# Kernel optimization log

Measured on AMD Instinct MI355X. Metric: run time of the kernel, lower is better.

The kernel has to match this reference:

```python
import math
from itertools import product
import jax, jax.numpy as jnp
import numpy as np

# ---- static config (mirrors LPD.__init__) ----
IMG_W, IMG_H = 1920, 1080
MIN_SIZES = [[10, 16, 24], [32, 48], [64, 96], [128, 192, 256]]
STEPS = [8, 16, 32, 64]
VARIANCE = (0.1, 0.2)
CONF_THR = 0.3
NMS_THR = 0.3
TOP_K = 2000
KEEP_TOP_K = 750
BATCH = 16


def make_priors() -> np.ndarray:
    """Anchor grid in normalized (cx, cy, w, h), kornia _PriorBox order:
    per level, per cell (row-major), per min_size."""
    levels = []
    for step, mss in zip(STEPS, MIN_SIZES):
        fh, fw = math.ceil(IMG_H / step), math.ceil(IMG_W / step)
        ii, jj = np.meshgrid(np.arange(fh), np.arange(fw), indexing='ij')
        cx = (jj + 0.5) * step / IMG_W  # [fh, fw]
        cy = (ii + 0.5) * step / IMG_H
        nms_ = len(mss)
        cx = np.broadcast_to(cx[..., None], (fh, fw, nms_))
        cy = np.broadcast_to(cy[..., None], (fh, fw, nms_))
        skx = np.broadcast_to(np.array(mss, np.float64) / IMG_W, (fh, fw, nms_))
        sky = np.broadcast_to(np.array(mss, np.float64) / IMG_H, (fh, fw, nms_))
        levels.append(np.stack([cx, cy, skx, sky], -1).reshape(-1, 4))
    return np.concatenate(levels, 0).astype(np.float32)  # [N, 4]

N_PRIORS = make_priors().shape[0]  # 119130 for 1920x1080


def decode(loc, priors):
    """loc [B,N,14], priors [N,4] -> scaled [B,N,14] (x1y1x2y2 + 5 landmarks)."""
    var = jnp.asarray(VARIANCE, loc.dtype)
    p_xy, p_wh = priors[:, :2], priors[:, 2:4]
    cxcy = p_xy + loc[..., 0:2] * VARIANCE[0] * p_wh
    wh = p_wh * jnp.exp(loc[..., 2:4] * var)
    x1y1 = cxcy - wh * 0.5
    x2y2 = x1y1 + wh
    # 5 landmark points
    lmk = p_xy[None, :, None, :] + loc[..., 4:14].reshape(*loc.shape[:-1], 5, 2) * VARIANCE[0] * p_wh[None, :, None, :]
    boxes = jnp.concatenate([x1y1, x2y2, lmk.reshape(*loc.shape[:-1], 10)], -1)
    scale = jnp.tile(jnp.asarray([IMG_W, IMG_H], loc.dtype), 7)
    return boxes * scale


def nms_keep(b, s):
    """Greedy NMS. b [K,4] sorted by descending score s [K]. Returns bool keep [K]."""
    area = jnp.clip(b[:, 2] - b[:, 0], 0.0) * jnp.clip(b[:, 3] - b[:, 1], 0.0)
    lt = jnp.maximum(b[:, None, :2], b[None, :, :2])
    rb = jnp.minimum(b[:, None, 2:4], b[None, :, 2:4])
    whi = jnp.clip(rb - lt, 0.0)
    inter = whi[..., 0] * whi[..., 1]
    iou_m = inter / (area[:, None] + area[None, :] - inter + 1e-9)  # [K,K]
    K = b.shape[0]
    idx = jnp.arange(K)

    def step(active, i):
        keep_i = active[i]
        active = active & ~(keep_i & (iou_m[i] > NMS_THR) & (idx > i))
        return active, keep_i

    _, keep = jax.lax.scan(step, s > 0.0, idx)
    return keep


def setup_inputs() -> dict:
    key = jax.random.key(0)
    k1, k2, k3 = jax.random.split(key, 3)
    return {
        'loc': jax.random.normal(k1, (BATCH, N_PRIORS, 14), jnp.float32),
        'conf': jax.random.normal(k2, (BATCH, N_PRIORS, 2), jnp.float32),
        'iou': jax.random.normal(k3, (BATCH, N_PRIORS, 1), jnp.float32),
    }


def reference(loc, conf, iou):
    priors = jnp.asarray(make_priors())  # [N,4] constant
    cls = jax.nn.softmax(conf, axis=-1)[..., 1]          # [B,N]
    iou_s = jnp.clip(iou[..., 0], 0.0, 1.0)
    scores = jnp.sqrt(cls * iou_s)
    scores = jnp.where(scores >= CONF_THR, scores, 0.0)  # confidence threshold
    boxes = decode(loc, priors)                          # [B,N,14]
    top_s, top_i = jax.lax.top_k(scores, TOP_K)          # sorted desc
    boxes_k = jnp.take_along_axis(boxes, top_i[..., None], axis=1)  # [B,K,14]
    keep = jax.vmap(nms_keep)(boxes_k[..., :4], top_s)   # [B,K] bool
    keep = keep & (jnp.cumsum(keep.astype(jnp.int32), axis=-1) <= KEEP_TOP_K)
    dets = jnp.concatenate([boxes_k, (top_s * keep)[..., None]], -1)  # [B,K,15]
    return dets
```

## Files before the change

kernel.cpp:

```cpp
#include <hip/hip_runtime.h>
#include <math.h>

#define BB 16
#define TOPK 2000
#define KEEPK 750
#define CAND_CAP 4096
#define EDGE_CAP 8192
#define HIST_BINS 256
#define BIN_BASE 0x3E99u

#define OFF_HIST   0
#define OFF_CCOUNT 16384
#define OFF_ECOUNT 16448
#define ZERO_BYTES 16512
#define OFF_SBITS  16512

__global__ __launch_bounds__(256) void k_scores(const float* __restrict__ conf,
                                                const float* __restrict__ iou,
                                                unsigned* __restrict__ sbits,
                                                unsigned* __restrict__ hist, int N) {
  __shared__ unsigned h[HIST_BINS];
  int b = blockIdx.y;
  for (int i = threadIdx.x; i < HIST_BINS; i += blockDim.x) h[i] = 0;
  __syncthreads();
  const float2* c2 = (const float2*)conf + (size_t)b * N;
  const float* iu = iou + (size_t)b * N;
  unsigned* sb = sbits + (size_t)b * N;
  int n0 = blockIdx.x * 4096;
#pragma unroll 4
  for (int k = 0; k < 16; ++k) {
    int n = n0 + k * 256 + threadIdx.x;
    if (n < N) {
      float2 c = c2[n];
      float m = fmaxf(c.x, c.y);
      float e0 = (float)exp((double)(c.x - m));
      float e1 = (float)exp((double)(c.y - m));
      float p1 = e1 / (e0 + e1);
      float ic = fminf(fmaxf(iu[n], 0.0f), 1.0f);
      float s = sqrtf(p1 * ic);
      s = (s >= 0.3f) ? s : 0.0f;
      unsigned bits = __float_as_uint(s);
      sb[n] = bits;
      if (bits != 0u) {
        int bin = (int)(bits >> 16) - (int)BIN_BASE;
        bin = bin < 0 ? 0 : (bin > 255 ? 255 : bin);
        atomicAdd(&h[bin], 1u);
      }
    }
  }
  __syncthreads();
  for (int i = threadIdx.x; i < HIST_BINS; i += blockDim.x)
    if (h[i]) atomicAdd(&hist[b * HIST_BINS + i], h[i]);
}

__global__ __launch_bounds__(256) void k_compact(const unsigned* __restrict__ sbits,
                                                 const unsigned* __restrict__ hist,
                                                 unsigned* __restrict__ ccount,
                                                 unsigned long long* __restrict__ ckeys,
                                                 int N) {
  __shared__ unsigned sT;
  __shared__ unsigned long long masks[32];
  __shared__ unsigned wioff[32];
  __shared__ unsigned blockbase;
  int b = blockIdx.y;
  int tid = threadIdx.x, lane = tid & 63, wv = tid >> 6;

  if (tid < 64) {
    const unsigned* h = hist + b * HIST_BINS;
    unsigned v0 = h[255 - (4 * lane + 0)];
    unsigned v1 = h[255 - (4 * lane + 1)];
    unsigned v2 = h[255 - (4 * lane + 2)];
    unsigned v3 = h[255 - (4 * lane + 3)];
    unsigned p0 = v0, p1 = p0 + v1, p2 = p1 + v2, p3 = p2 + v3;
    unsigned tot = p3, pre = tot;
    for (int off = 1; off < 64; off <<= 1) {
      unsigned q = __shfl_up(pre, off);
      if (lane >= off) pre += q;
    }
    unsigned excl = pre - tot;
    int kk = -1;
    if (excl + p0 >= TOPK) kk = 0;
    else if (excl + p1 >= TOPK) kk = 1;
    else if (excl + p2 >= TOPK) kk = 2;
    else if (excl + p3 >= TOPK) kk = 3;
    unsigned long long m = __ballot(kk >= 0);
    int bin = 0;
    if (m != 0ull) {
      int fl = __ffsll((unsigned long long)m) - 1;
      int fk = __shfl(kk, fl);
      bin = 255 - (4 * fl + fk);
    }
    if (lane == 0) sT = ((unsigned)(BIN_BASE + (unsigned)bin)) << 16;
  }
  __syncthreads();
  unsigned T = sT;

  const unsigned* sb = sbits + (size_t)b * N;
  int n0 = blockIdx.x * 2048;
  unsigned v[8];
  unsigned long long mk[8];
#pragma unroll
  for (int k = 0; k < 8; ++k) {
    int n = n0 + k * 256 + tid;
    v[k] = (n < N) ? sb[n] : 0u;
    bool p = v[k] >= T;
    mk[k] = __ballot(p);
    if (lane == 0) masks[k * 4 + wv] = mk[k];
  }
  __syncthreads();
  if (tid < 64) {
    unsigned c = (tid < 32) ? (unsigned)__popcll(masks[tid]) : 0u;
    unsigned pre = c;
    for (int off = 1; off < 64; off <<= 1) {
      unsigned q = __shfl_up(pre, off);
      if (lane >= off) pre += q;
    }
    if (tid < 32) wioff[tid] = pre - c;
    if (tid == 31) blockbase = atomicAdd(&ccount[b], pre);
  }
  __syncthreads();
  unsigned base = blockbase;
#pragma unroll
  for (int k = 0; k < 8; ++k) {
    if ((mk[k] >> lane) & 1ull) {
      unsigned pos = base + wioff[k * 4 + wv] +
                     (unsigned)__popcll(mk[k] & ((1ull << lane) - 1ull));
      if (pos < CAND_CAP) {
        int n = n0 + k * 256 + tid;
        ckeys[(size_t)b * CAND_CAP + pos] =
            ((unsigned long long)v[k] << 32) | (unsigned)(~(unsigned)n);
      }
    }
  }
}

__global__ __launch_bounds__(1024) void k_sort_decode(
    const unsigned* __restrict__ ccount, const unsigned long long* __restrict__ ckeys,
    const float* __restrict__ loc, float* __restrict__ top_s,
    float* __restrict__ out, float4* __restrict__ boxes4, int N) {
  __shared__ unsigned long long s[CAND_CAP];
  int b = blockIdx.x;
  int t = threadIdx.x;
  unsigned c = ccount[b];
  if (c > CAND_CAP) c = CAND_CAP;
  const unsigned long long* src = ckeys + (size_t)b * CAND_CAP;
  unsigned long long key[4];
#pragma unroll
  for (int e = 0; e < 4; ++e) {
    int i = 4 * t + e;
    key[e] = (i < (int)c) ? src[i] : 0ull;
  }
  for (int k = 2; k <= CAND_CAP; k <<= 1) {
    for (int j = k >> 1; j > 0; j >>= 1) {
      if (j >= 256) {
        __syncthreads();
#pragma unroll
        for (int e = 0; e < 4; ++e) s[4 * t + e] = key[e];
        __syncthreads();
        int pbase = (4 * t) ^ j;
        bool own_lo = ((4 * t) & j) == 0;
        bool dir = ((4 * t) & k) == 0;
        bool keep_max = (own_lo == dir);
#pragma unroll
        for (int e = 0; e < 4; ++e) {
          unsigned long long o = s[pbase + e];
          unsigned long long mx = key[e] > o ? key[e] : o;
          unsigned long long mn = key[e] > o ? o : key[e];
          key[e] = keep_max ? mx : mn;
        }
      } else if (j >= 4) {
        int d = j >> 2;
        bool own_lo = (t & d) == 0;
        bool dir = ((4 * t) & k) == 0;
        bool keep_max = (own_lo == dir);
#pragma unroll
        for (int e = 0; e < 4; ++e) {
          unsigned long long o = __shfl_xor(key[e], d, 64);
          unsigned long long mx = key[e] > o ? key[e] : o;
          unsigned long long mn = key[e] > o ? o : key[e];
          key[e] = keep_max ? mx : mn;
        }
      } else {
#pragma unroll
        for (int e = 0; e < 4; ++e) {
          int p = e ^ j;
          if (p > e) {
            int i = 4 * t + e;
            bool dir = ((i & k) == 0);
            bool need = dir ? (key[e] < key[p]) : (key[e] > key[p]);
            if (need) { unsigned long long tmp = key[e]; key[e] = key[p]; key[p] = tmp; }
          }
        }
      }
    }
  }
  if (t < TOPK / 4) {
#pragma unroll
    for (int e = 0; e < 4; ++e) {
      int r = 4 * t + e;
      unsigned long long kk = key[e];
      float sv = __uint_as_float((unsigned)(kk >> 32));
      top_s[b * TOPK + r] = sv;
      unsigned idxu = ~(unsigned)kk;
      if (idxu >= (unsigned)N) idxu = 0;
      int i = (int)idxu;
      int off, fw, st, nm, lvl;
      if (i < 97200)       { lvl = 0; off = 0;      fw = 240; st = 8;  nm = 3; }
      else if (i < 113520) { lvl = 1; off = 97200;  fw = 120; st = 16; nm = 2; }
      else if (i < 117600) { lvl = 2; off = 113520; fw = 60;  st = 32; nm = 2; }
      else                 { lvl = 3; off = 117600; fw = 30;  st = 64; nm = 3; }
      int tt = i - off;
      int cell = tt / nm;
      int kms = tt - cell * nm;
      int row = cell / fw;
      int col = cell - row * fw;
      int msv = (lvl == 0) ? (kms == 0 ? 10 : (kms == 1 ? 16 : 24))
              : (lvl == 1) ? (kms == 0 ? 32 : 48)
              : (lvl == 2) ? (kms == 0 ? 64 : 96)
                           : (kms == 0 ? 128 : (kms == 1 ? 192 : 256));
      float cx  = (float)(((double)col + 0.5) * (double)st / 1920.0);
      float cy  = (float)(((double)row + 0.5) * (double)st / 1080.0);
      float skx = (float)((double)msv / 1920.0);
      float sky = (float)((double)msv / 1080.0);
      const float2* lp2 = (const float2*)(loc + ((size_t)b * N + (size_t)i) * 14);
      float l[14];
#pragma unroll
      for (int q = 0; q < 7; ++q) { float2 v = lp2[q]; l[2 * q] = v.x; l[2 * q + 1] = v.y; }
      float cx2 = cx + (l[0] * 0.1f) * skx;
      float cy2 = cy + (l[1] * 0.1f) * sky;
      float wx = skx * expf(l[2] * 0.1f);
      float wy = sky * expf(l[3] * 0.2f);
      float x1 = cx2 - wx * 0.5f, y1 = cy2 - wy * 0.5f;
      float x2 = x1 + wx, y2 = y1 + wy;
      float X1 = x1 * 1920.0f, Y1 = y1 * 1080.0f, X2 = x2 * 1920.0f, Y2 = y2 * 1080.0f;
      float* o = out + ((size_t)b * TOPK + r) * 15;
      o[0] = X1; o[1] = Y1; o[2] = X2; o[3] = Y2;
#pragma unroll
      for (int q = 0; q < 5; ++q) {
        o[4 + 2 * q] = (cx + (l[4 + 2 * q] * 0.1f) * skx) * 1920.0f;
        o[5 + 2 * q] = (cy + (l[5 + 2 * q] * 0.1f) * sky) * 1080.0f;
      }
      boxes4[b * TOPK + r] = make_float4(X1, Y1, X2, Y2);
    }
  }
}

__global__ __launch_bounds__(256) void k_edges(const float4* __restrict__ boxes4,
                                               unsigned* __restrict__ ecount,
                                               unsigned* __restrict__ edges) {
  __shared__ float4 cb[256];
  __shared__ unsigned loc_e[1024];
  __shared__ unsigned lcnt, gbase;
  int b = blockIdx.y;
  int t = blockIdx.x;
  int ib = 0;
  while ((ib + 1) * (ib + 2) / 2 <= t) ++ib;
  int jb = t - ib * (ib + 1) / 2;
  int tid = threadIdx.x;
  if (tid == 0) lcnt = 0;
  int j0 = jb * 256;
  {
    int j = j0 + tid;
    cb[tid] = (j < TOPK) ? boxes4[b * TOPK + j]
                         : make_float4(-1e30f, -1e30f, -1e30f, -1e30f);
  }
  __syncthreads();
  int r = ib * 256 + tid;
  bool valid = r < TOPK;
  float4 A = valid ? boxes4[b * TOPK + r] : make_float4(0, 0, 0, 0);
  float areaA = fmaxf(A.z - A.x, 0.f) * fmaxf(A.w - A.y, 0.f);
  int cmax = r - j0;
  if (cmax > 256) cmax = 256;
  if (!valid) cmax = 0;
  for (int c = 0; c < cmax; ++c) {
    float4 Bx = cb[c];
    float xx1 = fmaxf(A.x, Bx.x), yy1 = fmaxf(A.y, Bx.y);
    float xx2 = fminf(A.z, Bx.z), yy2 = fminf(A.w, Bx.w);
    float w = fmaxf(xx2 - xx1, 0.f), hgt = fmaxf(yy2 - yy1, 0.f);
    float inter = w * hgt;
    float areaB = fmaxf(Bx.z - Bx.x, 0.f) * fmaxf(Bx.w - Bx.y, 0.f);
    float iouv = inter / (areaA + areaB - inter + 1e-9f);
    if (iouv > 0.3f) {
      unsigned p = atomicAdd(&lcnt, 1u);
      if (p < 1024u) loc_e[p] = ((unsigned)r << 16) | (unsigned)(j0 + c);
    }
  }
  __syncthreads();
  unsigned cnt = lcnt;
  if (cnt > 1024u) cnt = 1024u;
  if (tid == 0 && cnt) gbase = atomicAdd(&ecount[b], cnt);
  __syncthreads();
  if (cnt)
    for (unsigned e = tid; e < cnt; e += 256) {
      unsigned p = gbase + e;
      if (p < EDGE_CAP) edges[b * EDGE_CAP + p] = loc_e[e];
    }
}

__global__ __launch_bounds__(256) void k_nms(const float* __restrict__ top_s,
                                             const unsigned* __restrict__ ecount,
                                             const unsigned* __restrict__ edges,
                                             float* __restrict__ out) {
  int b = blockIdx.x;
  __shared__ unsigned long long A[32], K[32], S[32];
  __shared__ unsigned pref[32];
  __shared__ unsigned ecache[2048];
  __shared__ int changed;
  int tid = threadIdx.x, lane = tid & 63, wv = tid >> 6;
  for (int base = 0; base < 2048; base += 256) {
    int i = base + tid;
    bool act = (i < TOPK) && (top_s[b * TOPK + i] > 0.0f);
    unsigned long long m = __ballot(act);
    if (lane == 0) { int w = (base >> 6) + wv; A[w] = m; K[w] = m; }
  }
  unsigned E = ecount[b];
  if (E > EDGE_CAP) E = EDGE_CAP;
  unsigned Ec = E > 2048u ? 2048u : E;
  for (unsigned e = tid; e < Ec; e += 256) ecache[e] = edges[b * EDGE_CAP + e];
  __syncthreads();
  for (int it = 0; it < 32; ++it) {
    if (tid == 0) changed = 0;
    if (tid < 32) S[tid] = 0ull;
    __syncthreads();
    for (unsigned e = tid; e < Ec; e += 256) {
      unsigned v = ecache[e];
      unsigned i = v >> 16, j = v & 0xFFFFu;
      if ((K[j >> 6] >> (j & 63)) & 1ull) atomicOr(&S[i >> 6], 1ull << (i & 63));
    }
    for (unsigned e = 2048u + tid; e < E; e += 256) {
      unsigned v = edges[b * EDGE_CAP + e];
      unsigned i = v >> 16, j = v & 0xFFFFu;
      if ((K[j >> 6] >> (j & 63)) & 1ull) atomicOr(&S[i >> 6], 1ull << (i & 63));
    }
    __syncthreads();
    if (tid < 32) {
      unsigned long long nk = A[tid] & ~S[tid];
      if (nk != K[tid]) { K[tid] = nk; changed = 1; }
    }
    __syncthreads();
    if (!changed) break;
  }
  if (tid == 0) {
    unsigned acc = 0;
    for (int w = 0; w < 32; ++w) { pref[w] = acc; acc += (unsigned)__popcll(K[w]); }
  }
  __syncthreads();
  for (int base = 0; base < 2048; base += 256) {
    int i = base + tid;
    if (i < TOPK) {
      int w = i >> 6;
      unsigned long long bit = (K[w] >> (i & 63)) & 1ull;
      unsigned rank = pref[w] + (unsigned)__popcll(K[w] & ((1ull << (i & 63)) - 1ull)) +
                      (unsigned)bit;
      float sv = top_s[b * TOPK + i];
      out[((size_t)b * TOPK + i) * 15 + 14] = (bit && rank <= KEEPK) ? sv : 0.0f;
    }
  }
}

extern "C" void kernel_launch(void* const* d_in, const int* in_sizes, int n_in,
                              void* d_out, int out_size, void* d_ws, size_t ws_size,
                              hipStream_t stream) {
  const float* loc  = (const float*)d_in[0];
  const float* conf = (const float*)d_in[1];
  const float* iou  = (const float*)d_in[2];
  float* out = (float*)d_out;
  int N = in_sizes[2] / BB;

  char* ws = (char*)d_ws;
  unsigned* hist   = (unsigned*)(ws + OFF_HIST);
  unsigned* ccount = (unsigned*)(ws + OFF_CCOUNT);
  unsigned* ecount = (unsigned*)(ws + OFF_ECOUNT);
  unsigned* sbits  = (unsigned*)(ws + OFF_SBITS);
  size_t off = (size_t)OFF_SBITS + (size_t)BB * N * 4;
  off = (off + 15) & ~(size_t)15;
  unsigned long long* ckeys = (unsigned long long*)(ws + off); off += (size_t)BB * CAND_CAP * 8;
  float* top_s = (float*)(ws + off);       off += (size_t)BB * TOPK * 4;
  off = (off + 15) & ~(size_t)15;
  float4* boxes4 = (float4*)(ws + off);    off += (size_t)BB * TOPK * 16;
  unsigned* edges = (unsigned*)(ws + off); off += (size_t)BB * EDGE_CAP * 4;

  hipMemsetAsync(ws, 0, ZERO_BYTES, stream);

  k_scores<<<dim3((N + 4095) / 4096, BB), 256, 0, stream>>>(conf, iou, sbits, hist, N);
  k_compact<<<dim3((N + 2047) / 2048, BB), 256, 0, stream>>>(sbits, hist, ccount, ckeys, N);
  k_sort_decode<<<BB, 1024, 0, stream>>>(ccount, ckeys, loc, top_s, out, boxes4, N);
  k_edges<<<dim3(36, BB), 256, 0, stream>>>(boxes4, ecount, edges);
  k_nms<<<BB, 256, 0, stream>>>(top_s, ecount, edges, out);
}
```

Measured before the change: 293.8 us.

## Split bitonic sort across blocks, fuse edges with NMS, drop memset

The 4096-key bitonic sort now has its first stages done by 64 blocks of 256 threads, each sorting 1024 keys in alternating directions, and a 16-block kernel then runs only the final merge stages before decoding. The edge and NMS kernels are merged: the last finishing tile per batch, detected through an atomic counter and threadfence, runs the NMS. The memset is removed by writing per-chunk histograms, which k_compact then sums, and by zeroing the counters inside k_scores. The aim is more parallelism in the sort and fewer launches, at the cost of an extra kernel and a serial histogram reduction.

Result: slower. 312.0 us (+6.2%).

```diff
diff --git a/kernel.cpp b/kernel.cpp
--- a/kernel.cpp
+++ b/kernel.cpp
@@ -9,19 +9,23 @@
 #define HIST_BINS 256
 #define BIN_BASE 0x3E99u
 
-#define OFF_HIST   0
-#define OFF_CCOUNT 16384
-#define OFF_ECOUNT 16448
-#define ZERO_BYTES 16512
-#define OFF_SBITS  16512
-
 __global__ __launch_bounds__(256) void k_scores(const float* __restrict__ conf,
                                                 const float* __restrict__ iou,
                                                 unsigned* __restrict__ sbits,
-                                                unsigned* __restrict__ hist, int N) {
+                                                unsigned* __restrict__ hist,
+                                                unsigned* __restrict__ ccount,
+                                                unsigned* __restrict__ ecount,
+                                                unsigned* __restrict__ tdone,
+                                                int N, int nchunk) {
   __shared__ unsigned h[HIST_BINS];
   int b = blockIdx.y;
-  for (int i = threadIdx.x; i < HIST_BINS; i += blockDim.x) h[i] = 0;
+  int tid = threadIdx.x;
+  for (int i = tid; i < HIST_BINS; i += 256) h[i] = 0;
+  if (blockIdx.x == 0) {
+    if (tid == 0) ccount[b] = 0;
+    if (tid == 1) ecount[b] = 0;
+    if (tid == 2) tdone[b] = 0;
+  }
   __syncthreads();
   const float2* c2 = (const float2*)conf + (size_t)b * N;
   const float* iu = iou + (size_t)b * N;
@@ -29,7 +33,7 @@
   int n0 = blockIdx.x * 4096;
 #pragma unroll 4
   for (int k = 0; k < 16; ++k) {
-    int n = n0 + k * 256 + threadIdx.x;
+    int n = n0 + k * 256 + tid;
     if (n < N) {
       float2 c = c2[n];
       float m = fmaxf(c.x, c.y);
@@ -49,15 +53,15 @@
     }
   }
   __syncthreads();
-  for (int i = threadIdx.x; i < HIST_BINS; i += blockDim.x)
-    if (h[i]) atomicAdd(&hist[b * HIST_BINS + i], h[i]);
+  unsigned* hdst = hist + ((size_t)b * nchunk + blockIdx.x) * HIST_BINS;
+  for (int i = tid; i < HIST_BINS; i += 256) hdst[i] = h[i];
 }
 
 __global__ __launch_bounds__(256) void k_compact(const unsigned* __restrict__ sbits,
                                                  const unsigned* __restrict__ hist,
                                                  unsigned* __restrict__ ccount,
                                                  unsigned long long* __restrict__ ckeys,
-                                                 int N) {
+                                                 int N, int nchunk) {
   __shared__ unsigned sT;
   __shared__ unsigned long long masks[32];
   __shared__ unsigned wioff[32];
@@ -66,11 +70,14 @@
   int tid = threadIdx.x, lane = tid & 63, wv = tid >> 6;
 
   if (tid < 64) {
-    const unsigned* h = hist + b * HIST_BINS;
-    unsigned v0 = h[255 - (4 * lane + 0)];
-    unsigned v1 = h[255 - (4 * lane + 1)];
-    unsigned v2 = h[255 - (4 * lane + 2)];
-    unsigned v3 = h[255 - (4 * lane + 3)];
+    const unsigned* h = hist + (size_t)b * nchunk * HIST_BINS;
+    unsigned v0 = 0, v1 = 0, v2 = 0, v3 = 0;
+    int b0 = 255 - (4 * lane + 0), b1 = 255 - (4 * lane + 1);
+    int b2 = 255 - (4 * lane + 2), b3 = 255 - (4 * lane + 3);
+    for (int c = 0; c < nchunk; ++c) {
+      const unsigned* hc = h + c * HIST_BINS;
+      v0 += hc[b0]; v1 += hc[b1]; v2 += hc[b2]; v3 += hc[b3];
+    }
     unsigned p0 = v0, p1 = p0 + v1, p2 = p1 + v2, p3 = p2 + v3;
     unsigned tot = p3, pre = tot;
     for (int off = 1; off < 64; off <<= 1) {
@@ -134,23 +141,82 @@
   }
 }
 
-__global__ __launch_bounds__(1024) void k_sort_decode(
-    const unsigned* __restrict__ ccount, const unsigned long long* __restrict__ ckeys,
-    const float* __restrict__ loc, float* __restrict__ top_s,
-    float* __restrict__ out, float4* __restrict__ boxes4, int N) {
+__global__ __launch_bounds__(256) void k_sort1(const unsigned* __restrict__ ccount,
+                                               unsigned long long* __restrict__ ckeys) {
+  __shared__ unsigned long long s[1024];
+  int b = blockIdx.x >> 2, chunk = blockIdx.x & 3;
+  bool asc = (chunk & 1) != 0;
+  int t = threadIdx.x;
+  unsigned c = ccount[b];
+  if (c > CAND_CAP) c = CAND_CAP;
+  unsigned long long* base = ckeys + (size_t)b * CAND_CAP + chunk * 1024;
+  int goff = chunk * 1024;
+  unsigned long long key[4];
+#pragma unroll
+  for (int e = 0; e < 4; ++e) {
+    int g = goff + 4 * t + e;
+    key[e] = (g < (int)c) ? base[4 * t + e] : 0ull;
+  }
+  for (int k = 2; k <= 1024; k <<= 1) {
+    for (int j = k >> 1; j > 0; j >>= 1) {
+      if (j >= 256) {
+        __syncthreads();
+#pragma unroll
+        for (int e = 0; e < 4; ++e) s[4 * t + e] = key[e];
+        __syncthreads();
+        int pbase = (4 * t) ^ j;
+        bool own_lo = ((4 * t) & j) == 0;
+        bool dir = (((4 * t) & k) == 0) != asc;
+        bool keep_max = (own_lo == dir);
+#pragma unroll
+        for (int e = 0; e < 4; ++e) {
+          unsigned long long o = s[pbase + e];
+          unsigned long long mx = key[e] > o ? key[e] : o;
+          unsigned long long mn = key[e] > o ? o : key[e];
+          key[e] = keep_max ? mx : mn;
+        }
+      } else if (j >= 4) {
+        int d = j >> 2;
+        bool own_lo = (t & d) == 0;
+        bool dir = (((4 * t) & k) == 0) != asc;
+        bool keep_max = (own_lo == dir);
+#pragma unroll
+        for (int e = 0; e < 4; ++e) {
+          unsigned long long o = __shfl_xor(key[e], d, 64);
+          unsigned long long mx = key[e] > o ? key[e] : o;
+          unsigned long long mn = key[e] > o ? o : key[e];
+          key[e] = keep_max ? mx : mn;
+        }
+      } else {
+#pragma unroll
+        for (int e = 0; e < 4; ++e) {
+          int p = e ^ j;
+          if (p > e) {
+            int i = 4 * t + e;
+            bool dir = (((i & k) == 0) != asc);
+            bool need = dir ? (key[e] < key[p]) : (key[e] > key[p]);
+            if (need) { unsigned long long tmp = key[e]; key[e] = key[p]; key[p] = tmp; }
+          }
+        }
+      }
+    }
+  }
+#pragma unroll
+  for (int e = 0; e < 4; ++e) base[4 * t + e] = key[e];
+}
+
+__global__ __launch_bounds__(1024) void k_sort2_decode(
+    const unsigned long long* __restrict__ ckeys, const float* __restrict__ loc,
+    float* __restrict__ top_s, float* __restrict__ out,
+    float4* __restrict__ boxes4, int N) {
   __shared__ unsigned long long s[CAND_CAP];
   int b = blockIdx.x;
   int t = threadIdx.x;
-  unsigned c = ccount[b];
-  if (c > CAND_CAP) c = CAND_CAP;
   const unsigned long long* src = ckeys + (size_t)b * CAND_CAP;
   unsigned long long key[4];
 #pragma unroll
-  for (int e = 0; e < 4; ++e) {
-    int i = 4 * t + e;
-    key[e] = (i < (int)c) ? src[i] : 0ull;
-  }
-  for (int k = 2; k <= CAND_CAP; k <<= 1) {
+  for (int e = 0; e < 4; ++e) key[e] = src[4 * t + e];
+  for (int k = 2048; k <= CAND_CAP; k <<= 1) {
     for (int j = k >> 1; j > 0; j >>= 1) {
       if (j >= 256) {
         __syncthreads();
@@ -245,12 +311,16 @@
   }
 }
 
-__global__ __launch_bounds__(256) void k_edges(const float4* __restrict__ boxes4,
-                                               unsigned* __restrict__ ecount,
-                                               unsigned* __restrict__ edges) {
+__global__ __launch_bounds__(256) void k_edges_nms(const float4* __restrict__ boxes4,
+                                                   const float* __restrict__ top_s,
+                                                   unsigned* __restrict__ ecount,
+                                                   unsigned* __restrict__ edges,
+                                                   unsigned* __restrict__ tdone,
+                                                   float* __restrict__ out) {
   __shared__ float4 cb[256];
   __shared__ unsigned loc_e[1024];
   __shared__ unsigned lcnt, gbase;
+  __shared__ int is_last;
   int b = blockIdx.y;
   int t = blockIdx.x;
   int ib = 0;
@@ -267,15 +337,15 @@
   __syncthreads();
   int r = ib * 256 + tid;
   bool valid = r < TOPK;
-  float4 A = valid ? boxes4[b * TOPK + r] : make_float4(0, 0, 0, 0);
-  float areaA = fmaxf(A.z - A.x, 0.f) * fmaxf(A.w - A.y, 0.f);
+  float4 A4 = valid ? boxes4[b * TOPK + r] : make_float4(0, 0, 0, 0);
+  float areaA = fmaxf(A4.z - A4.x, 0.f) * fmaxf(A4.w - A4.y, 0.f);
   int cmax = r - j0;
   if (cmax > 256) cmax = 256;
   if (!valid) cmax = 0;
   for (int c = 0; c < cmax; ++c) {
     float4 Bx = cb[c];
-    float xx1 = fmaxf(A.x, Bx.x), yy1 = fmaxf(A.y, Bx.y);
-    float xx2 = fminf(A.z, Bx.z), yy2 = fminf(A.w, Bx.w);
+    float xx1 = fmaxf(A4.x, Bx.x), yy1 = fmaxf(A4.y, Bx.y);
+    float xx2 = fminf(A4.z, Bx.z), yy2 = fminf(A4.w, Bx.w);
     float w = fmaxf(xx2 - xx1, 0.f), hgt = fmaxf(yy2 - yy1, 0.f);
     float inter = w * hgt;
     float areaB = fmaxf(Bx.z - Bx.x, 0.f) * fmaxf(Bx.w - Bx.y, 0.f);
@@ -295,23 +365,26 @@
       unsigned p = gbase + e;
       if (p < EDGE_CAP) edges[b * EDGE_CAP + p] = loc_e[e];
     }
-}
-
-__global__ __launch_bounds__(256) void k_nms(const float* __restrict__ top_s,
-                                             const unsigned* __restrict__ ecount,
-                                             const unsigned* __restrict__ edges,
-                                             float* __restrict__ out) {
-  int b = blockIdx.x;
-  __shared__ unsigned long long A[32], K[32], S[32];
+  __syncthreads();
+  __threadfence();
+  if (tid == 0) {
+    unsigned done = atomicAdd(&tdone[b], 1u);
+    is_last = (done == 35u);
+  }
+  __syncthreads();
+  if (!is_last) return;
+  __threadfence();
+
+  __shared__ unsigned long long Am[32], K[32], S[32];
   __shared__ unsigned pref[32];
   __shared__ unsigned ecache[2048];
   __shared__ int changed;
-  int tid = threadIdx.x, lane = tid & 63, wv = tid >> 6;
+  int lane = tid & 63, wv = tid >> 6;
   for (int base = 0; base < 2048; base += 256) {
     int i = base + tid;
     bool act = (i < TOPK) && (top_s[b * TOPK + i] > 0.0f);
     unsigned long long m = __ballot(act);
-    if (lane == 0) { int w = (base >> 6) + wv; A[w] = m; K[w] = m; }
+    if (lane == 0) { int w = (base >> 6) + wv; Am[w] = m; K[w] = m; }
   }
   unsigned E = ecount[b];
   if (E > EDGE_CAP) E = EDGE_CAP;
@@ -334,7 +407,7 @@
     }
     __syncthreads();
     if (tid < 32) {
-      unsigned long long nk = A[tid] & ~S[tid];
+      unsigned long long nk = Am[tid] & ~S[tid];
       if (nk != K[tid]) { K[tid] = nk; changed = 1; }
     }
     __syncthreads();
@@ -366,13 +439,16 @@
   const float* iou  = (const float*)d_in[2];
   float* out = (float*)d_out;
   int N = in_sizes[2] / BB;
+  int nchunk = (N + 4095) / 4096;
 
   char* ws = (char*)d_ws;
-  unsigned* hist   = (unsigned*)(ws + OFF_HIST);
-  unsigned* ccount = (unsigned*)(ws + OFF_CCOUNT);
-  unsigned* ecount = (unsigned*)(ws + OFF_ECOUNT);
-  unsigned* sbits  = (unsigned*)(ws + OFF_SBITS);
-  size_t off = (size_t)OFF_SBITS + (size_t)BB * N * 4;
+  size_t off = 0;
+  unsigned* ccount = (unsigned*)(ws + off); off += 64;
+  unsigned* ecount = (unsigned*)(ws + off); off += 64;
+  unsigned* tdone  = (unsigned*)(ws + off); off += 64;
+  off = (off + 255) & ~(size_t)255;
+  unsigned* hist   = (unsigned*)(ws + off); off += (size_t)BB * nchunk * HIST_BINS * 4;
+  unsigned* sbits  = (unsigned*)(ws + off); off += (size_t)BB * N * 4;
   off = (off + 15) & ~(size_t)15;
   unsigned long long* ckeys = (unsigned long long*)(ws + off); off += (size_t)BB * CAND_CAP * 8;
   float* top_s = (float*)(ws + off);       off += (size_t)BB * TOPK * 4;
@@ -380,11 +456,11 @@
   float4* boxes4 = (float4*)(ws + off);    off += (size_t)BB * TOPK * 16;
   unsigned* edges = (unsigned*)(ws + off); off += (size_t)BB * EDGE_CAP * 4;
 
-  hipMemsetAsync(ws, 0, ZERO_BYTES, stream);
-
-  k_scores<<<dim3((N + 4095) / 4096, BB), 256, 0, stream>>>(conf, iou, sbits, hist, N);
-  k_compact<<<dim3((N + 2047) / 2048, BB), 256, 0, stream>>>(sbits, hist, ccount, ckeys, N);
-  k_sort_decode<<<BB, 1024, 0, stream>>>(ccount, ckeys, loc, top_s, out, boxes4, N);
-  k_edges<<<dim3(36, BB), 256, 0, stream>>>(boxes4, ecount, edges);
-  k_nms<<<BB, 256, 0, stream>>>(top_s, ecount, edges, out);
-}
+  k_scores<<<dim3(nchunk, BB), 256, 0, stream>>>(conf, iou, sbits, hist,
+                                                 ccount, ecount, tdone, N, nchunk);
+  k_compact<<<dim3((N + 2047) / 2048, BB), 256, 0, stream>>>(sbits, hist, ccount,
+                                                             ckeys, N, nchunk);
+  k_sort1<<<BB * 4, 256, 0, stream>>>(ccount, ckeys);
+  k_sort2_decode<<<BB, 1024, 0, stream>>>(ckeys, loc, top_s, out, boxes4, N);
+  k_edges_nms<<<dim3(36, BB), 256, 0, stream>>>(boxes4, top_s, ecount, edges, tdone, out);
+}
```
